# Optimization experiments

Hardware: AMD Instinct MI355X
Metric: run time of the kernel (lower is better)

Reference implementation:

```python
import jax, jax.numpy as jnp
import numpy as np

SEQ_LEN = 4_194_304  # number of tokens
INPUT_BITS = 16      # bits per token, MSB first


def setup_inputs() -> dict:
    key = jax.random.key(0)
    # bits in {0,1}; float32 carrier (values exact, matches uint8 bit semantics)
    tokens = jax.random.randint(key, (SEQ_LEN, INPUT_BITS), 0, 2).astype(jnp.float32)
    return {"tokens": tokens}


def reference(tokens):
    # tokens: [seq_len, input_bits], MSB first, entries in {0,1}
    bits = tokens.shape[1]
    # _bits_to_int: val = val*2 + b  ==  dot with [2^(bits-1), ..., 2, 1]
    pow2 = jnp.exp2(jnp.arange(bits - 1, -1, -1, dtype=jnp.float32))  # [bits]
    values = tokens @ pow2  # [seq_len], exact for bits <= 24
    # stable ascending sort == Python list.sort on (value, original_index)
    order = jnp.argsort(values, stable=True)  # [seq_len]
    return tokens[order]  # gather rows by rank
```

## Files before the change

### kernel.cpp

```cpp
#include <hip/hip_runtime.h>
#include <stdint.h>

static constexpr uint32_t SEQN = 4194304u;
static constexpr uint32_t BINS = 65536u;
static constexpr uint32_t QWORDS = BINS / 4u;
static constexpr uint32_t NBLK = 512u;
static constexpr uint32_t NTHR = 1024u;
static constexpr uint32_t ROWS_PER_BLK = SEQN / NBLK;

__global__ __launch_bounds__(NTHR) void k_hist_lds(const float4* __restrict__ in4,
                                                   uint32_t* __restrict__ partial) {
  __shared__ uint32_t h[QWORDS];
  uint32_t tid = threadIdx.x, blk = blockIdx.x;
  uint4* hv = (uint4*)h;
  for (uint32_t i = tid; i < QWORDS / 4u; i += NTHR) hv[i] = make_uint4(0u, 0u, 0u, 0u);
  __syncthreads();
  uint32_t q = tid & 3u;
  uint32_t shift = 12u - (q << 2);
  bool leader = (q == 0u);
  const float4* base = in4 + (size_t)blk * (ROWS_PER_BLK * 4u);
#pragma unroll 8
  for (uint32_t t = 0; t < (ROWS_PER_BLK * 4u) / NTHR; ++t) {
    float4 v = base[(size_t)t * NTHR + tid];
    float nf = ((v.x * 2.0f + v.y) * 2.0f + v.z) * 2.0f + v.w;
    uint32_t part = ((uint32_t)nf) << shift;
    part += __shfl_xor(part, 1, 64);
    part += __shfl_xor(part, 2, 64);
    if (leader) atomicAdd(&h[part >> 2], 1u << ((part & 3u) << 3));
  }
  __syncthreads();
  uint4* dst = (uint4*)(partial + (size_t)blk * QWORDS);
  for (uint32_t i = tid; i < QWORDS / 4u; i += NTHR) dst[i] = hv[i];
}

__global__ __launch_bounds__(NTHR) void k_reduceB(const uint32_t* __restrict__ partial,
                                                  uint32_t* __restrict__ hist,
                                                  uint32_t* __restrict__ blkTot) {
  __shared__ uint2 acc[4][256];
  __shared__ uint32_t wt[4];
  uint32_t tid = threadIdx.x, blk = blockIdx.x;
  uint32_t wl = tid & 255u, g = tid >> 8;
  uint32_t w = blk * 256u + wl;
  uint32_t e = 0u, o = 0u;
  uint32_t p0 = g * (NBLK / 4u);
#pragma unroll 8
  for (uint32_t p = p0; p < p0 + NBLK / 4u; ++p) {
    uint32_t v = partial[(size_t)p * QWORDS + w];
    e += v & 0x00FF00FFu;
    o += (v >> 8) & 0x00FF00FFu;
  }
  acc[g][wl] = make_uint2(e, o);
  __syncthreads();
  if (g == 0u) {
    uint2 a1 = acc[1][wl], a2 = acc[2][wl], a3 = acc[3][wl];
    e += a1.x + a2.x + a3.x;
    o += a1.y + a2.y + a3.y;
    uint32_t c0 = e & 0xFFFFu, c2 = e >> 16, c1 = o & 0xFFFFu, c3 = o >> 16;
    ((uint4*)hist)[w] = make_uint4(c0, c1, c2, c3);
    uint32_t ssum = c0 + c1 + c2 + c3;
    for (int d = 1; d < 64; d <<= 1) ssum += __shfl_xor(ssum, d, 64);
    if ((tid & 63u) == 0u) wt[tid >> 6] = ssum;
  }
  __syncthreads();
  if (tid == 0u) blkTot[blk] = wt[0] + wt[1] + wt[2] + wt[3];
}

__global__ __launch_bounds__(256) void k_zero(uint32_t* __restrict__ hist) {
  uint32_t i = blockIdx.x * 256u + threadIdx.x;
  if (i < BINS) hist[i] = 0u;
}

__global__ __launch_bounds__(256) void k_hist(const float4* __restrict__ in4,
                                              uint32_t* __restrict__ hist) {
  uint32_t r = blockIdx.x * 256u + threadIdx.x;
  if (r >= SEQN) return;
  uint32_t key = 0u;
#pragma unroll
  for (uint32_t qq = 0; qq < 4u; ++qq) {
    float4 v = in4[(size_t)r * 4u + qq];
    uint32_t nib = ((uint32_t)v.x << 3) | ((uint32_t)v.y << 2) |
                   ((uint32_t)v.z << 1) | (uint32_t)v.w;
    key = (key << 4) | nib;
  }
  atomicAdd(&hist[key], 1u);
}

__global__ __launch_bounds__(256) void k_scan1(const uint32_t* __restrict__ hist,
                                               uint32_t* __restrict__ blkTot) {
  uint32_t tid = threadIdx.x, blk = blockIdx.x;
  uint32_t b0 = blk * 1024u + tid * 4u;
  uint32_t s = hist[b0] + hist[b0 + 1] + hist[b0 + 2] + hist[b0 + 3];
  for (int d = 1; d < 64; d <<= 1) s += __shfl_xor(s, d, 64);
  __shared__ uint32_t wt[4];
  if ((tid & 63u) == 0u) wt[tid >> 6] = s;
  __syncthreads();
  if (tid == 0u) blkTot[blk] = wt[0] + wt[1] + wt[2] + wt[3];
}

__global__ __launch_bounds__(256) void k_scanB(const uint32_t* __restrict__ hist,
                                               const uint32_t* __restrict__ blkTot,
                                               uint32_t* __restrict__ offs) {
  __shared__ uint32_t s_base;
  __shared__ uint32_t wt[4];
  uint32_t tid = threadIdx.x, blk = blockIdx.x;
  if (tid < 64u) {
    uint32_t v = blkTot[tid];
    uint32_t incl = v;
    for (int d = 1; d < 64; d <<= 1) {
      uint32_t n = __shfl_up(incl, d, 64);
      if (tid >= (uint32_t)d) incl += n;
    }
    if (tid == blk) s_base = incl - v;
  }
  __syncthreads();
  uint32_t lane = tid & 63u, wid = tid >> 6;
  uint32_t b0 = blk * 1024u + tid * 4u;
  uint4 c = ((const uint4*)hist)[b0 >> 2];
  uint32_t s = c.x + c.y + c.z + c.w;
  uint32_t incl = s;
  for (int d = 1; d < 64; d <<= 1) {
    uint32_t n = __shfl_up(incl, d, 64);
    if (lane >= (uint32_t)d) incl += n;
  }
  if (lane == 63u) wt[wid] = incl;
  __syncthreads();
  uint32_t wbase = 0u;
  for (uint32_t w = 0; w < wid; ++w) wbase += wt[w];
  uint32_t base = s_base + wbase + (incl - s);
  ((uint4*)offs)[b0 >> 2] = make_uint4(base, base + c.x, base + c.x + c.y,
                                       base + c.x + c.y + c.z);
}

__global__ __launch_bounds__(256) void k_write(const uint32_t* __restrict__ hist,
                                               const uint32_t* __restrict__ offs,
                                               float4* __restrict__ out4) {
  __shared__ uint32_t s_off[32], s_cnt[32];
  uint32_t tid = threadIdx.x, blk = blockIdx.x;
  if (tid < 32u) {
    uint32_t k = blk * 32u + tid;
    s_off[tid] = offs[k];
    s_cnt[tid] = hist[k];
  }
  __syncthreads();
  uint32_t lane = tid & 63u, wid = tid >> 6;
  uint32_t q = lane & 3u;
  for (uint32_t kk = 0; kk < 8u; ++kk) {
    uint32_t ki = wid * 8u + kk;
    uint32_t k = blk * 32u + ki;
    uint32_t off = s_off[ki], cnt = s_cnt[ki];
    float4 pat;
    pat.x = (float)((k >> (15u - (q * 4u + 0u))) & 1u);
    pat.y = (float)((k >> (15u - (q * 4u + 1u))) & 1u);
    pat.z = (float)((k >> (15u - (q * 4u + 2u))) & 1u);
    pat.w = (float)((k >> (15u - (q * 4u + 3u))) & 1u);
    size_t base = (size_t)off * 4u;
    uint32_t tot = cnt * 4u;
    for (uint32_t j = lane; j < tot; j += 64u) out4[base + j] = pat;
  }
}

extern "C" void kernel_launch(void* const* d_in, const int* in_sizes, int n_in,
                              void* d_out, int out_size, void* d_ws, size_t ws_size,
                              hipStream_t stream) {
  const float4* in4 = (const float4*)d_in[0];
  float4* out4 = (float4*)d_out;
  uint32_t* hist = (uint32_t*)d_ws;
  uint32_t* offs = hist + BINS;
  uint32_t* blkTot = offs + BINS;
  uint32_t* partial = blkTot + 1024u;

  size_t need = ((size_t)2 * BINS + 1024u + (size_t)NBLK * QWORDS) * 4u;
  if (ws_size >= need) {
    k_hist_lds<<<NBLK, NTHR, 0, stream>>>(in4, partial);
    k_reduceB<<<64, NTHR, 0, stream>>>(partial, hist, blkTot);
  } else {
    k_zero<<<BINS / 256, 256, 0, stream>>>(hist);
    k_hist<<<SEQN / 256, 256, 0, stream>>>(in4, hist);
    k_scan1<<<64, 256, 0, stream>>>(hist, blkTot);
  }
  k_scanB<<<64, 256, 0, stream>>>(hist, blkTot, offs);
  k_write<<<BINS / 32, 256, 0, stream>>>(hist, offs, out4);
}
```

Measured before the change: 143.2 us.

## Fuse histogram, scan and scatter into one cooperative kernel with nontemporal stores

Combines the per-block LDS histogram, the partial reduction, the offset scan and the output fill into a single cooperative kernel separated by grid-wide syncs. The write phase is remapped to 512 blocks handling 128 keys each, and output stores become nontemporal. This removes several kernel launches and the gaps between them, at the cost of grid barriers and the requirement that all blocks be co-resident. The fallback for a small workspace is dropped, so in that case nothing is launched.

```diff
diff --git a/kernel.cpp b/kernel.cpp
--- a/kernel.cpp
+++ b/kernel.cpp
@@ -1,5 +1,8 @@
 #include <hip/hip_runtime.h>
+#include <hip/hip_cooperative_groups.h>
 #include <stdint.h>
+
+namespace cg = cooperative_groups;
 
 static constexpr uint32_t SEQN = 4194304u;
 static constexpr uint32_t BINS = 65536u;
@@ -8,9 +11,143 @@
 static constexpr uint32_t NTHR = 1024u;
 static constexpr uint32_t ROWS_PER_BLK = SEQN / NBLK;
 
+typedef float vfloat4 __attribute__((ext_vector_type(4)));
+
+__device__ __forceinline__ void nt_store4(float4* p, float x, float y, float z, float w) {
+  vfloat4 v = {x, y, z, w};
+  __builtin_nontemporal_store(v, (vfloat4*)p);
+}
+
+__global__ __launch_bounds__(NTHR, 8) void k_fused(const float4* __restrict__ in4,
+                                                   float4* __restrict__ out4,
+                                                   uint32_t* __restrict__ partial,
+                                                   uint32_t* __restrict__ hist,
+                                                   uint32_t* __restrict__ offs,
+                                                   uint32_t* __restrict__ blkTot) {
+  __shared__ __align__(16) uint32_t h[QWORDS];
+  __shared__ uint32_t wt[4];
+  __shared__ uint32_t c_base;
+  cg::grid_group grid = cg::this_grid();
+  uint32_t tid = threadIdx.x, blk = blockIdx.x;
+
+  {
+    uint4* hv = (uint4*)h;
+    for (uint32_t i = tid; i < QWORDS / 4u; i += NTHR) hv[i] = make_uint4(0u, 0u, 0u, 0u);
+    __syncthreads();
+    uint32_t q = tid & 3u;
+    uint32_t shift = 12u - (q << 2);
+    bool leader = (q == 0u);
+    const float4* base = in4 + (size_t)blk * (ROWS_PER_BLK * 4u);
+#pragma unroll 8
+    for (uint32_t t = 0; t < (ROWS_PER_BLK * 4u) / NTHR; ++t) {
+      float4 v = base[(size_t)t * NTHR + tid];
+      float nf = ((v.x * 2.0f + v.y) * 2.0f + v.z) * 2.0f + v.w;
+      uint32_t part = ((uint32_t)nf) << shift;
+      part += __shfl_xor(part, 1, 64);
+      part += __shfl_xor(part, 2, 64);
+      if (leader) atomicAdd(&h[part >> 2], 1u << ((part & 3u) << 3));
+    }
+    __syncthreads();
+    uint4* dst = (uint4*)(partial + (size_t)blk * QWORDS);
+    for (uint32_t i = tid; i < QWORDS / 4u; i += NTHR) dst[i] = hv[i];
+  }
+  grid.sync();
+
+  if (blk < 64u) {
+    uint2* acc2 = (uint2*)h;
+    uint32_t wl = tid & 255u, g = tid >> 8;
+    uint32_t w = blk * 256u + wl;
+    uint32_t e = 0u, o = 0u;
+    uint32_t p0 = g * (NBLK / 4u);
+#pragma unroll 8
+    for (uint32_t p = p0; p < p0 + NBLK / 4u; ++p) {
+      uint32_t v = partial[(size_t)p * QWORDS + w];
+      e += v & 0x00FF00FFu;
+      o += (v >> 8) & 0x00FF00FFu;
+    }
+    acc2[g * 256u + wl] = make_uint2(e, o);
+    __syncthreads();
+    if (g == 0u) {
+      uint2 a1 = acc2[256u + wl], a2 = acc2[512u + wl], a3 = acc2[768u + wl];
+      e += a1.x + a2.x + a3.x;
+      o += a1.y + a2.y + a3.y;
+      uint32_t c0 = e & 0xFFFFu, c2 = e >> 16, c1 = o & 0xFFFFu, c3 = o >> 16;
+      ((uint4*)hist)[w] = make_uint4(c0, c1, c2, c3);
+      uint32_t ssum = c0 + c1 + c2 + c3;
+      for (int d = 1; d < 64; d <<= 1) ssum += __shfl_xor(ssum, d, 64);
+      if ((tid & 63u) == 0u) wt[tid >> 6] = ssum;
+    }
+    __syncthreads();
+    if (tid == 0u) blkTot[blk] = wt[0] + wt[1] + wt[2] + wt[3];
+  }
+  grid.sync();
+
+  if (blk < 64u && tid < 64u) {
+    uint32_t v = blkTot[tid];
+    uint32_t incl = v;
+    for (int d = 1; d < 64; d <<= 1) {
+      uint32_t n = __shfl_up(incl, d, 64);
+      if (tid >= (uint32_t)d) incl += n;
+    }
+    if (tid == blk) c_base = incl - v;
+  }
+  __syncthreads();
+  uint32_t c_s = 0u, c_incl = 0u;
+  uint4 c_c = make_uint4(0u, 0u, 0u, 0u);
+  if (blk < 64u && tid < 256u) {
+    uint32_t lane = tid & 63u;
+    uint32_t b0 = blk * 1024u + tid * 4u;
+    c_c = ((const uint4*)hist)[b0 >> 2];
+    c_s = c_c.x + c_c.y + c_c.z + c_c.w;
+    c_incl = c_s;
+    for (int d = 1; d < 64; d <<= 1) {
+      uint32_t n = __shfl_up(c_incl, d, 64);
+      if (lane >= (uint32_t)d) c_incl += n;
+    }
+    if (lane == 63u) wt[tid >> 6] = c_incl;
+  }
+  __syncthreads();
+  if (blk < 64u && tid < 256u) {
+    uint32_t wid = tid >> 6;
+    uint32_t wbase = 0u;
+    for (uint32_t w = 0; w < wid; ++w) wbase += wt[w];
+    uint32_t base = c_base + wbase + (c_incl - c_s);
+    uint32_t b0 = blk * 1024u + tid * 4u;
+    ((uint4*)offs)[b0 >> 2] = make_uint4(base, base + c_c.x, base + c_c.x + c_c.y,
+                                         base + c_c.x + c_c.y + c_c.z);
+  }
+  grid.sync();
+
+  {
+    uint32_t* s_off = h;
+    uint32_t* s_cnt = h + 128u;
+    if (tid < 128u) {
+      uint32_t k = blk * 128u + tid;
+      s_off[tid] = offs[k];
+      s_cnt[tid] = hist[k];
+    }
+    __syncthreads();
+    uint32_t lane = tid & 63u, wid = tid >> 6;
+    uint32_t q = lane & 3u;
+    for (uint32_t kk = 0; kk < 8u; ++kk) {
+      uint32_t ki = wid * 8u + kk;
+      uint32_t k = blk * 128u + ki;
+      uint32_t off = s_off[ki], cnt = s_cnt[ki];
+      float px = (float)((k >> (15u - (q * 4u + 0u))) & 1u);
+      float py = (float)((k >> (15u - (q * 4u + 1u))) & 1u);
+      float pz = (float)((k >> (15u - (q * 4u + 2u))) & 1u);
+      float pw = (float)((k >> (15u - (q * 4u + 3u))) & 1u);
+      size_t base = (size_t)off * 4u;
+      uint32_t tot = cnt * 4u;
+      for (uint32_t j = lane; j < tot; j += 64u)
+        nt_store4(&out4[base + j], px, py, pz, pw);
+    }
+  }
+}
+
 __global__ __launch_bounds__(NTHR) void k_hist_lds(const float4* __restrict__ in4,
                                                    uint32_t* __restrict__ partial) {
-  __shared__ uint32_t h[QWORDS];
+  __shared__ __align__(16) uint32_t h[QWORDS];
   uint32_t tid = threadIdx.x, blk = blockIdx.x;
   uint4* hv = (uint4*)h;
   for (uint32_t i = tid; i < QWORDS / 4u; i += NTHR) hv[i] = make_uint4(0u, 0u, 0u, 0u);
@@ -65,38 +202,6 @@
   if (tid == 0u) blkTot[blk] = wt[0] + wt[1] + wt[2] + wt[3];
 }
 
-__global__ __launch_bounds__(256) void k_zero(uint32_t* __restrict__ hist) {
-  uint32_t i = blockIdx.x * 256u + threadIdx.x;
-  if (i < BINS) hist[i] = 0u;
-}
-
-__global__ __launch_bounds__(256) void k_hist(const float4* __restrict__ in4,
-                                              uint32_t* __restrict__ hist) {
-  uint32_t r = blockIdx.x * 256u + threadIdx.x;
-  if (r >= SEQN) return;
-  uint32_t key = 0u;
-#pragma unroll
-  for (uint32_t qq = 0; qq < 4u; ++qq) {
-    float4 v = in4[(size_t)r * 4u + qq];
-    uint32_t nib = ((uint32_t)v.x << 3) | ((uint32_t)v.y << 2) |
-                   ((uint32_t)v.z << 1) | (uint32_t)v.w;
-    key = (key << 4) | nib;
-  }
-  atomicAdd(&hist[key], 1u);
-}
-
-__global__ __launch_bounds__(256) void k_scan1(const uint32_t* __restrict__ hist,
-                                               uint32_t* __restrict__ blkTot) {
-  uint32_t tid = threadIdx.x, blk = blockIdx.x;
-  uint32_t b0 = blk * 1024u + tid * 4u;
-  uint32_t s = hist[b0] + hist[b0 + 1] + hist[b0 + 2] + hist[b0 + 3];
-  for (int d = 1; d < 64; d <<= 1) s += __shfl_xor(s, d, 64);
-  __shared__ uint32_t wt[4];
-  if ((tid & 63u) == 0u) wt[tid >> 6] = s;
-  __syncthreads();
-  if (tid == 0u) blkTot[blk] = wt[0] + wt[1] + wt[2] + wt[3];
-}
-
 __global__ __launch_bounds__(256) void k_scanB(const uint32_t* __restrict__ hist,
                                                const uint32_t* __restrict__ blkTot,
                                                uint32_t* __restrict__ offs) {
@@ -148,14 +253,14 @@
     uint32_t ki = wid * 8u + kk;
     uint32_t k = blk * 32u + ki;
     uint32_t off = s_off[ki], cnt = s_cnt[ki];
-    float4 pat;
-    pat.x = (float)((k >> (15u - (q * 4u + 0u))) & 1u);
-    pat.y = (float)((k >> (15u - (q * 4u + 1u))) & 1u);
-    pat.z = (float)((k >> (15u - (q * 4u + 2u))) & 1u);
-    pat.w = (float)((k >> (15u - (q * 4u + 3u))) & 1u);
+    float px = (float)((k >> (15u - (q * 4u + 0u))) & 1u);
+    float py = (float)((k >> (15u - (q * 4u + 1u))) & 1u);
+    float pz = (float)((k >> (15u - (q * 4u + 2u))) & 1u);
+    float pw = (float)((k >> (15u - (q * 4u + 3u))) & 1u);
     size_t base = (size_t)off * 4u;
     uint32_t tot = cnt * 4u;
-    for (uint32_t j = lane; j < tot; j += 64u) out4[base + j] = pat;
+    for (uint32_t j = lane; j < tot; j += 64u)
+      nt_store4(&out4[base + j], px, py, pz, pw);
   }
 }
 
@@ -170,14 +275,18 @@
   uint32_t* partial = blkTot + 1024u;
 
   size_t need = ((size_t)2 * BINS + 1024u + (size_t)NBLK * QWORDS) * 4u;
+  bool coop_ok = false;
   if (ws_size >= need) {
+    void* args[] = {(void*)&in4, (void*)&out4, (void*)&partial,
+                    (void*)&hist, (void*)&offs, (void*)&blkTot};
+    hipError_t err = hipLaunchCooperativeKernel((const void*)k_fused, dim3(NBLK),
+                                                dim3(NTHR), args, 0, stream);
+    coop_ok = (err == hipSuccess);
+  }
+  if (!coop_ok && ws_size >= need) {
     k_hist_lds<<<NBLK, NTHR, 0, stream>>>(in4, partial);
     k_reduceB<<<64, NTHR, 0, stream>>>(partial, hist, blkTot);
-  } else {
-    k_zero<<<BINS / 256, 256, 0, stream>>>(hist);
-    k_hist<<<SEQN / 256, 256, 0, stream>>>(in4, hist);
-    k_scan1<<<64, 256, 0, stream>>>(hist, blkTot);
-  }
-  k_scanB<<<64, 256, 0, stream>>>(hist, blkTot, offs);
-  k_write<<<BINS / 32, 256, 0, stream>>>(hist, offs, out4);
-}
+    k_scanB<<<64, 256, 0, stream>>>(hist, blkTot, offs);
+    k_write<<<BINS / 32, 256, 0, stream>>>(hist, offs, out4);
+  }
+}
```

Result: slower. 289.4 us (+102.1%).

## Stage histogram input via async global-to-LDS loads and split reduction finer

Applied to the files above, without the earlier changes.

The LDS histogram kernel now prefetches input rows into a double-buffered LDS staging area with global_load_lds and waits on vmcnt, so loads overlap with the atomic binning. The block count is halved to 256, which halves the partial histograms the reducer must read. The reduce step is split into 256 smaller blocks that accumulate block totals with atomics, with the totals zeroed at the start of the histogram kernel. This uses 64KB of extra LDS per block and relies on correct ordering of the zeroing and the atomics across kernels.

```diff
diff --git a/kernel.cpp b/kernel.cpp
--- a/kernel.cpp
+++ b/kernel.cpp
@@ -4,43 +4,71 @@
 static constexpr uint32_t SEQN = 4194304u;
 static constexpr uint32_t BINS = 65536u;
 static constexpr uint32_t QWORDS = BINS / 4u;
-static constexpr uint32_t NBLK = 512u;
+static constexpr uint32_t NBLK = 256u;
 static constexpr uint32_t NTHR = 1024u;
 static constexpr uint32_t ROWS_PER_BLK = SEQN / NBLK;
+static constexpr uint32_t ITERS = 32u;
+
+__device__ __forceinline__ void gload16(const float4* g, uint32_t* lds) {
+  __builtin_amdgcn_global_load_lds(
+      (const __attribute__((address_space(1))) void*)g,
+      (__attribute__((address_space(3))) void*)lds, 16, 0, 0);
+}
 
 __global__ __launch_bounds__(NTHR) void k_hist_lds(const float4* __restrict__ in4,
-                                                   uint32_t* __restrict__ partial) {
-  __shared__ uint32_t h[QWORDS];
-  uint32_t tid = threadIdx.x, blk = blockIdx.x;
+                                                   uint32_t* __restrict__ partial,
+                                                   uint32_t* __restrict__ blkTot) {
+  __shared__ __align__(16) uint32_t h[QWORDS];
+  __shared__ __align__(16) uint32_t stage[16384];
+  uint32_t tid = threadIdx.x, blk = blockIdx.x;
+  uint32_t lane = tid & 63u, wid = tid >> 6;
+  if (blk == 0u && tid < 64u) blkTot[tid] = 0u;
   uint4* hv = (uint4*)h;
   for (uint32_t i = tid; i < QWORDS / 4u; i += NTHR) hv[i] = make_uint4(0u, 0u, 0u, 0u);
   __syncthreads();
-  uint32_t q = tid & 3u;
+
+  uint32_t q = lane & 3u;
   uint32_t shift = 12u - (q << 2);
   bool leader = (q == 0u);
-  const float4* base = in4 + (size_t)blk * (ROWS_PER_BLK * 4u);
-#pragma unroll 8
-  for (uint32_t t = 0; t < (ROWS_PER_BLK * 4u) / NTHR; ++t) {
-    float4 v = base[(size_t)t * NTHR + tid];
-    float nf = ((v.x * 2.0f + v.y) * 2.0f + v.z) * 2.0f + v.w;
-    uint32_t part = ((uint32_t)nf) << shift;
-    part += __shfl_xor(part, 1, 64);
-    part += __shfl_xor(part, 2, 64);
-    if (leader) atomicAdd(&h[part >> 2], 1u << ((part & 3u) << 3));
+  const float4* gbase = in4 + ((size_t)blk * 65536u + (size_t)wid * 4096u);
+  uint32_t* sbase = stage + wid * 1024u;
+
+  gload16(gbase + lane, sbase);
+  gload16(gbase + 64u + lane, sbase + 256u);
+
+  for (uint32_t t = 0; t < ITERS; ++t) {
+    if (t + 1u < ITERS) {
+      const float4* gp = gbase + (size_t)(t + 1u) * 128u;
+      uint32_t* sp = sbase + ((t + 1u) & 1u) * 512u;
+      gload16(gp + lane, sp);
+      gload16(gp + 64u + lane, sp + 256u);
+      asm volatile("s_waitcnt vmcnt(2)" ::: "memory");
+    } else {
+      asm volatile("s_waitcnt vmcnt(0)" ::: "memory");
+    }
+    uint32_t* cb = sbase + (t & 1u) * 512u;
+#pragma unroll
+    for (uint32_t r = 0; r < 2u; ++r) {
+      float4 v = *(const float4*)(cb + r * 256u + lane * 4u);
+      float nf = ((v.x * 2.0f + v.y) * 2.0f + v.z) * 2.0f + v.w;
+      uint32_t part = ((uint32_t)nf) << shift;
+      part += __shfl_xor(part, 1, 64);
+      part += __shfl_xor(part, 2, 64);
+      if (leader) atomicAdd(&h[part >> 2], 1u << ((part & 3u) << 3));
+    }
   }
   __syncthreads();
   uint4* dst = (uint4*)(partial + (size_t)blk * QWORDS);
   for (uint32_t i = tid; i < QWORDS / 4u; i += NTHR) dst[i] = hv[i];
 }
 
-__global__ __launch_bounds__(NTHR) void k_reduceB(const uint32_t* __restrict__ partial,
-                                                  uint32_t* __restrict__ hist,
-                                                  uint32_t* __restrict__ blkTot) {
-  __shared__ uint2 acc[4][256];
-  __shared__ uint32_t wt[4];
-  uint32_t tid = threadIdx.x, blk = blockIdx.x;
-  uint32_t wl = tid & 255u, g = tid >> 8;
-  uint32_t w = blk * 256u + wl;
+__global__ __launch_bounds__(256) void k_reduceC(const uint32_t* __restrict__ partial,
+                                                 uint32_t* __restrict__ hist,
+                                                 uint32_t* __restrict__ blkTot) {
+  __shared__ uint2 acc[4][64];
+  uint32_t tid = threadIdx.x, b = blockIdx.x;
+  uint32_t wl = tid & 63u, g = tid >> 6;
+  uint32_t w = b * 64u + wl;
   uint32_t e = 0u, o = 0u;
   uint32_t p0 = g * (NBLK / 4u);
 #pragma unroll 8
@@ -59,15 +87,15 @@
     ((uint4*)hist)[w] = make_uint4(c0, c1, c2, c3);
     uint32_t ssum = c0 + c1 + c2 + c3;
     for (int d = 1; d < 64; d <<= 1) ssum += __shfl_xor(ssum, d, 64);
-    if ((tid & 63u) == 0u) wt[tid >> 6] = ssum;
-  }
-  __syncthreads();
-  if (tid == 0u) blkTot[blk] = wt[0] + wt[1] + wt[2] + wt[3];
-}
-
-__global__ __launch_bounds__(256) void k_zero(uint32_t* __restrict__ hist) {
+    if (wl == 0u) atomicAdd(&blkTot[b >> 2], ssum);
+  }
+}
+
+__global__ __launch_bounds__(256) void k_zero(uint32_t* __restrict__ hist,
+                                              uint32_t* __restrict__ blkTot) {
   uint32_t i = blockIdx.x * 256u + threadIdx.x;
   if (i < BINS) hist[i] = 0u;
+  if (i < 64u) blkTot[i] = 0u;
 }
 
 __global__ __launch_bounds__(256) void k_hist(const float4* __restrict__ in4,
@@ -171,10 +199,10 @@
 
   size_t need = ((size_t)2 * BINS + 1024u + (size_t)NBLK * QWORDS) * 4u;
   if (ws_size >= need) {
-    k_hist_lds<<<NBLK, NTHR, 0, stream>>>(in4, partial);
-    k_reduceB<<<64, NTHR, 0, stream>>>(partial, hist, blkTot);
+    k_hist_lds<<<NBLK, NTHR, 0, stream>>>(in4, partial, blkTot);
+    k_reduceC<<<256, 256, 0, stream>>>(partial, hist, blkTot);
   } else {
-    k_zero<<<BINS / 256, 256, 0, stream>>>(hist);
+    k_zero<<<BINS / 256, 256, 0, stream>>>(hist, blkTot);
     k_hist<<<SEQN / 256, 256, 0, stream>>>(in4, hist);
     k_scan1<<<64, 256, 0, stream>>>(hist, blkTot);
   }
```

New measurement: 149.3 us. 1.04x slower.
